# Kernel tuning notes

Measured on AMD Instinct MI355X. Metric: run time of the kernel, lower is better.

Reference implementation:

```python
import jax, jax.numpy as jnp
import numpy as np

B, T, C, H = 2, 2048, 1024, 16
HD = C // H  # head dim = 64


def setup_inputs() -> dict:
    key = jax.random.key(0)
    ks = jax.random.split(key, 5)
    s = 0.02
    return {
        "x": jax.random.normal(ks[0], (B, T, C), dtype=jnp.float32),
        "w_attn": jax.random.normal(ks[1], (C, 3 * C), dtype=jnp.float32) * s,
        "b_attn": jnp.zeros((3 * C,), dtype=jnp.float32),
        "w_proj": jax.random.normal(ks[2], (C, C), dtype=jnp.float32) * s,
        "b_proj": jnp.zeros((C,), dtype=jnp.float32),
    }


def reference(x, w_attn, b_attn, w_proj, b_proj):
    Bc, Tc, Cc = x.shape
    qkv = x @ w_attn + b_attn                      # [B,T,3C]
    q, k, v = jnp.split(qkv, 3, axis=2)            # each [B,T,C]
    # [B,T,C] -> [B,H,T,HD]
    def heads(t):
        return t.reshape(Bc, Tc, H, HD).transpose(0, 2, 1, 3)
    q, k, v = heads(q), heads(k), heads(v)
    scale = 1.0 / jnp.sqrt(jnp.asarray(HD, dtype=x.dtype))
    att = jnp.einsum("bhqd,bhkd->bhqk", q, k) * scale   # [B,H,T,T]
    causal = jnp.tril(jnp.ones((Tc, Tc), dtype=bool))
    att = jnp.where(causal, att, jnp.asarray(-jnp.inf, dtype=att.dtype))
    att = jax.nn.softmax(att, axis=-1)
    y = jnp.einsum("bhqk,bhkd->bhqd", att, v)            # [B,H,T,HD]
    y = y.transpose(0, 2, 1, 3).reshape(Bc, Tc, Cc)      # [B,T,C]
    return y @ w_proj + b_proj
```

## Files before the change

kernel.cpp:

```cpp
#include <hip/hip_runtime.h>
#include <stdint.h>


typedef short bf16x8 __attribute__((ext_vector_type(8)));
typedef float f32x4 __attribute__((ext_vector_type(4)));

__device__ inline unsigned short f2bf(float f) {
  union { float f; uint32_t u; } v; v.f = f;
  uint32_t u = v.u;
  u += 0x7FFFu + ((u >> 16) & 1u);
  return (unsigned short)(u >> 16);
}

__device__ inline unsigned pkbf(float a, float b) {
  unsigned r;
  asm("v_cvt_pk_bf16_f32 %0, %1, %2" : "=v"(r) : "v"(a), "v"(b));
  return r;
}

__device__ inline float exp2_fast(float x) {
#if __has_builtin(__builtin_amdgcn_exp2f)
  return __builtin_amdgcn_exp2f(x);
#else
  float r; asm("v_exp_f32 %0, %1" : "=v"(r) : "v"(x)); return r;
#endif
}

__device__ inline void load_lds16(const unsigned short* g, unsigned short* l) {
  __builtin_amdgcn_global_load_lds(
      (const __attribute__((address_space(1))) unsigned int*)(const void*)g,
      (__attribute__((address_space(3))) unsigned int*)(void*)l, 16, 0, 0);
}

__global__ __launch_bounds__(256) void prep_kernel(
    const float* __restrict__ x, const float* __restrict__ w_attn,
    const float* __restrict__ w_proj,
    unsigned short* __restrict__ xb, unsigned short* __restrict__ wattnT,
    unsigned short* __restrict__ wprojT) {
  __shared__ float tile[32][33];
  const int b = blockIdx.x, t = threadIdx.x;
  if (b < 4096) {
    int i = b * 256 + t;
    float4 f = reinterpret_cast<const float4*>(x)[i];
    ushort4 o;
    o.x = f2bf(f.x); o.y = f2bf(f.y); o.z = f2bf(f.z); o.w = f2bf(f.w);
    reinterpret_cast<ushort4*>(xb)[i] = o;
    return;
  }
  const float* in; unsigned short* out; int R, Cn, bx, by;
  if (b < 7168) {
    int bb = b - 4096;
    in = w_attn; out = wattnT; R = 1024; Cn = 3072;
    bx = (bb % 96) * 32; by = (bb / 96) * 32;
  } else {
    int bb = b - 7168;
    in = w_proj; out = wprojT; R = 1024; Cn = 1024;
    bx = (bb % 32) * 32; by = (bb / 32) * 32;
  }
  const int tx = t & 31, ty = t >> 5;
  #pragma unroll
  for (int i = 0; i < 32; i += 8)
    tile[ty + i][tx] = in[(size_t)(by + ty + i) * Cn + bx + tx];
  __syncthreads();
  #pragma unroll
  for (int i = 0; i < 32; i += 8)
    out[(size_t)(bx + ty + i) * R + by + tx] = f2bf(tile[tx][ty + i]);
}

__global__ __launch_bounds__(256) void gemm_bt64_kernel(
    const unsigned short* __restrict__ A,
    const unsigned short* __restrict__ Bt,
    const float* __restrict__ bias,
    void* __restrict__ outp,
    unsigned short* __restrict__ vtp,
    int M, int N, int K, int mode) {
  __shared__ unsigned short As[2][128 * 64];
  __shared__ unsigned short Bs[2][128 * 64];
  const int t = threadIdx.x;
  const int wave = t >> 6, lane = t & 63;
  const int L = lane & 15, quad = lane >> 4;
  const int wm = (wave >> 1) * 64, wn = (wave & 1) * 64;
  const int m0 = blockIdx.y * 128, n0 = blockIdx.x * 128;

  const int drow = lane >> 3;
  const int dch  = (lane & 7) ^ drow;
  const int fo0 = ((quad ^ (L & 7)) * 8);
  const int fo1 = (((quad + 4) ^ (L & 7)) * 8);

  const unsigned short* Ab = A  + (size_t)(m0 + wave * 32 + drow) * K + dch * 8;
  const unsigned short* Bb = Bt + (size_t)(n0 + wave * 32 + drow) * K + dch * 8;

  f32x4 acc[4][4] = {};
  const int NK2 = K >> 6;

  #pragma unroll
  for (int j = 0; j < 4; ++j) {
    int r0 = wave * 32 + j * 8;
    load_lds16(Ab + (size_t)j * 8 * K, &As[0][r0 * 64]);
    load_lds16(Bb + (size_t)j * 8 * K, &Bs[0][r0 * 64]);
  }

  int buf = 0;
  for (int kt = 0; kt < NK2; ++kt) {
    asm volatile("" ::: "memory");
    __builtin_amdgcn_s_waitcnt(0x0F70);
    __builtin_amdgcn_s_barrier();
    asm volatile("" ::: "memory");

    if (kt + 1 < NK2) {
      #pragma unroll
      for (int j = 0; j < 4; ++j) {
        int r0 = wave * 32 + j * 8;
        load_lds16(Ab + (size_t)j * 8 * K + (size_t)(kt + 1) * 64, &As[buf ^ 1][r0 * 64]);
        load_lds16(Bb + (size_t)j * 8 * K + (size_t)(kt + 1) * 64, &Bs[buf ^ 1][r0 * 64]);
      }
    }

    bf16x8 af[4], bf[4];
    #pragma unroll
    for (int mt = 0; mt < 4; ++mt)
      af[mt] = *reinterpret_cast<const bf16x8*>(&As[buf][(wm + mt * 16 + L) * 64 + fo0]);
    #pragma unroll
    for (int nt = 0; nt < 4; ++nt)
      bf[nt] = *reinterpret_cast<const bf16x8*>(&Bs[buf][(wn + nt * 16 + L) * 64 + fo0]);
    __builtin_amdgcn_s_setprio(1);
    #pragma unroll
    for (int mt = 0; mt < 4; ++mt)
      #pragma unroll
      for (int nt = 0; nt < 4; ++nt)
        acc[mt][nt] = __builtin_amdgcn_mfma_f32_16x16x32_bf16(af[mt], bf[nt], acc[mt][nt], 0, 0, 0);
    __builtin_amdgcn_s_setprio(0);

    #pragma unroll
    for (int mt = 0; mt < 4; ++mt)
      af[mt] = *reinterpret_cast<const bf16x8*>(&As[buf][(wm + mt * 16 + L) * 64 + fo1]);
    #pragma unroll
    for (int nt = 0; nt < 4; ++nt)
      bf[nt] = *reinterpret_cast<const bf16x8*>(&Bs[buf][(wn + nt * 16 + L) * 64 + fo1]);
    __builtin_amdgcn_s_setprio(1);
    #pragma unroll
    for (int mt = 0; mt < 4; ++mt)
      #pragma unroll
      for (int nt = 0; nt < 4; ++nt)
        acc[mt][nt] = __builtin_amdgcn_mfma_f32_16x16x32_bf16(af[mt], bf[nt], acc[mt][nt], 0, 0, 0);
    __builtin_amdgcn_s_setprio(0);
    buf ^= 1;
  }

  if (mode == 0) {
    float* out = (float*)outp;
    #pragma unroll
    for (int mt = 0; mt < 4; ++mt)
      #pragma unroll
      for (int nt = 0; nt < 4; ++nt) {
        int col = n0 + wn + nt * 16 + L;
        float b = bias[col];
        #pragma unroll
        for (int r = 0; r < 4; ++r) {
          int row = m0 + wm + mt * 16 + quad * 4 + r;
          out[(size_t)row * N + col] = acc[mt][nt][r] + b;
        }
      }
  } else {
    unsigned short* qkv = (unsigned short*)outp;
    #pragma unroll
    for (int mt = 0; mt < 4; ++mt)
      #pragma unroll
      for (int nt = 0; nt < 4; ++nt) {
        int col = n0 + wn + nt * 16 + L;
        int sel = col >> 10, cc = col & 1023;
        int h = cc >> 6, d = cc & 63;
        float b = bias[col];
        float sc = (sel == 0) ? 0.18033688011112042f : 1.0f;
        #pragma unroll
        for (int r = 0; r < 4; ++r) {
          int row = m0 + wm + mt * 16 + quad * 4 + r;
          int bb = row >> 11, tt = row & 2047;
          float val = (acc[mt][nt][r] + b) * sc;
          if (sel == 2) {
            vtp[((size_t)(bb * 16 + h) * 64 + d) * 2048 + tt] = f2bf(val);
          } else {
            qkv[(((size_t)sel * 32 + (size_t)(bb * 16 + h)) * 2048 + tt) * 64 + d] = f2bf(val);
          }
        }
      }
  }
}

template<int BM, int BN>
__global__ __launch_bounds__(256) void gemm_bt_kernel(
    const unsigned short* __restrict__ A,
    const unsigned short* __restrict__ Bt,
    const float* __restrict__ bias,
    float* __restrict__ out,
    int M, int N, int K) {
  constexpr int MT = BM / 32, NT = BN / 32;
  constexpr int RPWA = BM / 4, RPWB = BN / 4;
  constexpr int NJA = RPWA / 16, NJB = RPWB / 16;
  __shared__ unsigned short As[2][BM * 32];
  __shared__ unsigned short Bs[2][BN * 32];
  const int t = threadIdx.x;
  const int wave = t >> 6, lane = t & 63;
  const int L = lane & 15, quad = lane >> 4;
  const int wm = (wave >> 1) * (BM / 2), wn = (wave & 1) * (BN / 2);
  const int m0 = blockIdx.y * BM, n0 = blockIdx.x * BN;

  const int drow = lane >> 2;
  const int dch  = (lane & 3) ^ ((drow >> 1) & 3);
  const int foff = ((quad ^ ((L >> 1) & 3)) * 8);

  const unsigned short* Ab = A  + (size_t)(m0 + wave * RPWA + drow) * K + dch * 8;
  const unsigned short* Bb = Bt + (size_t)(n0 + wave * RPWB + drow) * K + dch * 8;

  f32x4 acc[MT][NT] = {};
  const int NK = K >> 5;

  #pragma unroll
  for (int j = 0; j < NJA; ++j)
    load_lds16(Ab + (size_t)j * 16 * K, &As[0][(wave * RPWA + j * 16) * 32]);
  #pragma unroll
  for (int j = 0; j < NJB; ++j)
    load_lds16(Bb + (size_t)j * 16 * K, &Bs[0][(wave * RPWB + j * 16) * 32]);

  int buf = 0;
  for (int kt = 0; kt < NK; ++kt) {
    asm volatile("" ::: "memory");
    __builtin_amdgcn_s_waitcnt(0x0F70);
    __builtin_amdgcn_s_barrier();
    asm volatile("" ::: "memory");

    if (kt + 1 < NK) {
      #pragma unroll
      for (int j = 0; j < NJA; ++j)
        load_lds16(Ab + (size_t)j * 16 * K + (kt + 1) * 32,
                   &As[buf ^ 1][(wave * RPWA + j * 16) * 32]);
      #pragma unroll
      for (int j = 0; j < NJB; ++j)
        load_lds16(Bb + (size_t)j * 16 * K + (kt + 1) * 32,
                   &Bs[buf ^ 1][(wave * RPWB + j * 16) * 32]);
    }

    bf16x8 af[MT], bf[NT];
    #pragma unroll
    for (int mt = 0; mt < MT; ++mt)
      af[mt] = *reinterpret_cast<const bf16x8*>(&As[buf][(wm + mt * 16 + L) * 32 + foff]);
    #pragma unroll
    for (int nt = 0; nt < NT; ++nt)
      bf[nt] = *reinterpret_cast<const bf16x8*>(&Bs[buf][(wn + nt * 16 + L) * 32 + foff]);
    __builtin_amdgcn_s_setprio(1);
    #pragma unroll
    for (int mt = 0; mt < MT; ++mt)
      #pragma unroll
      for (int nt = 0; nt < NT; ++nt)
        acc[mt][nt] = __builtin_amdgcn_mfma_f32_16x16x32_bf16(af[mt], bf[nt], acc[mt][nt], 0, 0, 0);
    __builtin_amdgcn_s_setprio(0);
    buf ^= 1;
  }

  #pragma unroll
  for (int mt = 0; mt < MT; ++mt)
    #pragma unroll
    for (int nt = 0; nt < NT; ++nt) {
      int col = n0 + wn + nt * 16 + L;
      float b = bias[col];
      #pragma unroll
      for (int r = 0; r < 4; ++r) {
        int row = m0 + wm + mt * 16 + quad * 4 + r;
        out[(size_t)row * N + col] = acc[mt][nt][r] + b;
      }
    }
}

__global__ __launch_bounds__(256) void attn_kernel(
    const unsigned short* __restrict__ qkv,
    const unsigned short* __restrict__ vt,
    unsigned short* __restrict__ y) {
  __shared__ unsigned short Ks[3][64 * 64];
  __shared__ unsigned short Vs[3][64 * 64];
  __shared__ unsigned short Ps[4][32][72];

  const int t = threadIdx.x;
  const int wave = t >> 6, lane = t & 63;
  const int L = lane & 15, quad = lane >> 4;
  const int b = blockIdx.x;
  const int bh = (b & 7) * 4 + ((b >> 3) & 3);
  const int pi = b >> 5;
  const int tA = pi, tB = 31 - pi;
  const int rowA0 = tA * 64 + wave * 16;
  const int rowB0 = tB * 64 + wave * 16;
  const int ntiles = tB + 1;

  const unsigned short* qb  = qkv + ((size_t)bh * 2048) * 64;
  const unsigned short* kb  = qkv + ((size_t)(32 + bh) * 2048) * 64;
  const unsigned short* vtb = vt + (size_t)bh * 64 * 2048;

  const int drow = lane >> 3;
  const int dch  = (lane & 7) ^ drow;
  const int fo0 = ((quad ^ (L & 7)) * 8);
  const int fo1 = (((quad + 4) ^ (L & 7)) * 8);

  bf16x8 qfA[2], qfB[2];
  #pragma unroll
  for (int h = 0; h < 2; ++h) {
    qfA[h] = *reinterpret_cast<const bf16x8*>(qb + (size_t)(rowA0 + L) * 64 + h * 32 + quad * 8);
    qfB[h] = *reinterpret_cast<const bf16x8*>(qb + (size_t)(rowB0 + L) * 64 + h * 32 + quad * 8);
  }

  f32x4 oA[4] = {}, oB[4] = {};
  float rsA = 0.f, rsB = 0.f;

  {
    #pragma unroll
    for (int j = 0; j < 2; ++j) {
      int r0 = wave * 16 + j * 8;
      load_lds16(kb  + (size_t)(0 + r0 + drow) * 64 + dch * 8, &Ks[0][r0 * 64]);
      load_lds16(vtb + (size_t)(r0 + drow) * 2048 + 0 + dch * 8, &Vs[0][r0 * 64]);
    }
  }

  int buf = 0;
  for (int kt = 0; kt < ntiles; ++kt) {
    const int nkt = (kt + 1 < ntiles) ? kt + 1 : ntiles - 1;
    const int nbuf = (buf == 2) ? 0 : buf + 1;
    {
      const int kg = nkt * 64;
      #pragma unroll
      for (int j = 0; j < 2; ++j) {
        int r0 = wave * 16 + j * 8;
        load_lds16(kb  + (size_t)(kg + r0 + drow) * 64 + dch * 8, &Ks[nbuf][r0 * 64]);
        load_lds16(vtb + (size_t)(r0 + drow) * 2048 + kg + dch * 8, &Vs[nbuf][r0 * 64]);
      }
    }
    asm volatile("" ::: "memory");
    __builtin_amdgcn_s_waitcnt(0x0F74);
    __builtin_amdgcn_s_barrier();
    asm volatile("" ::: "memory");

    const bool actA = (kt <= tA);

    bf16x8 kf[4][2];
    #pragma unroll
    for (int nt = 0; nt < 4; ++nt) {
      kf[nt][0] = *reinterpret_cast<const bf16x8*>(&Ks[buf][(nt * 16 + L) * 64 + fo0]);
      kf[nt][1] = *reinterpret_cast<const bf16x8*>(&Ks[buf][(nt * 16 + L) * 64 + fo1]);
    }

    f32x4 sB[4] = {};
    __builtin_amdgcn_s_setprio(1);
    #pragma unroll
    for (int nt = 0; nt < 4; ++nt) {
      sB[nt] = __builtin_amdgcn_mfma_f32_16x16x32_bf16(kf[nt][0], qfB[0], sB[nt], 0, 0, 0);
      sB[nt] = __builtin_amdgcn_mfma_f32_16x16x32_bf16(kf[nt][1], qfB[1], sB[nt], 0, 0, 0);
    }
    __builtin_amdgcn_s_setprio(0);
    if (kt == tB) {
      #pragma unroll
      for (int nt = 0; nt < 4; ++nt) {
        int key0 = kt * 64 + nt * 16 + quad * 4;
        int qr = rowB0 + L;
        #pragma unroll
        for (int r = 0; r < 4; ++r)
          if (key0 + r > qr) sB[nt][r] = -3.0e38f;
      }
    }
    #pragma unroll
    for (int nt = 0; nt < 4; ++nt) {
      float p0 = exp2_fast(sB[nt][0]), p1 = exp2_fast(sB[nt][1]);
      float p2 = exp2_fast(sB[nt][2]), p3 = exp2_fast(sB[nt][3]);
      rsB += (p0 + p1) + (p2 + p3);
      uint2 pk;
      pk.x = pkbf(p0, p1);
      pk.y = pkbf(p2, p3);
      *reinterpret_cast<uint2*>(&Ps[wave][16 + L][nt * 16 + quad * 4]) = pk;
    }

    if (actA) {
      f32x4 sA[4] = {};
      __builtin_amdgcn_s_setprio(1);
      #pragma unroll
      for (int nt = 0; nt < 4; ++nt) {
        sA[nt] = __builtin_amdgcn_mfma_f32_16x16x32_bf16(kf[nt][0], qfA[0], sA[nt], 0, 0, 0);
        sA[nt] = __builtin_amdgcn_mfma_f32_16x16x32_bf16(kf[nt][1], qfA[1], sA[nt], 0, 0, 0);
      }
      __builtin_amdgcn_s_setprio(0);
      if (kt == tA) {
        #pragma unroll
        for (int nt = 0; nt < 4; ++nt) {
          int key0 = kt * 64 + nt * 16 + quad * 4;
          int qr = rowA0 + L;
          #pragma unroll
          for (int r = 0; r < 4; ++r)
            if (key0 + r > qr) sA[nt][r] = -3.0e38f;
        }
      }
      #pragma unroll
      for (int nt = 0; nt < 4; ++nt) {
        float p0 = exp2_fast(sA[nt][0]), p1 = exp2_fast(sA[nt][1]);
        float p2 = exp2_fast(sA[nt][2]), p3 = exp2_fast(sA[nt][3]);
        rsA += (p0 + p1) + (p2 + p3);
        uint2 pk;
        pk.x = pkbf(p0, p1);
        pk.y = pkbf(p2, p3);
        *reinterpret_cast<uint2*>(&Ps[wave][L][nt * 16 + quad * 4]) = pk;
      }
    }

    bf16x8 vf[4][2];
    #pragma unroll
    for (int nt = 0; nt < 4; ++nt) {
      vf[nt][0] = *reinterpret_cast<const bf16x8*>(&Vs[buf][(nt * 16 + L) * 64 + fo0]);
      vf[nt][1] = *reinterpret_cast<const bf16x8*>(&Vs[buf][(nt * 16 + L) * 64 + fo1]);
    }
    bf16x8 pb0 = *reinterpret_cast<const bf16x8*>(&Ps[wave][16 + L][quad * 8]);
    bf16x8 pb1 = *reinterpret_cast<const bf16x8*>(&Ps[wave][16 + L][32 + quad * 8]);
    __builtin_amdgcn_s_setprio(1);
    #pragma unroll
    for (int nt = 0; nt < 4; ++nt) {
      oB[nt] = __builtin_amdgcn_mfma_f32_16x16x32_bf16(pb0, vf[nt][0], oB[nt], 0, 0, 0);
      oB[nt] = __builtin_amdgcn_mfma_f32_16x16x32_bf16(pb1, vf[nt][1], oB[nt], 0, 0, 0);
    }
    __builtin_amdgcn_s_setprio(0);
    if (actA) {
      bf16x8 pa0 = *reinterpret_cast<const bf16x8*>(&Ps[wave][L][quad * 8]);
      bf16x8 pa1 = *reinterpret_cast<const bf16x8*>(&Ps[wave][L][32 + quad * 8]);
      __builtin_amdgcn_s_setprio(1);
      #pragma unroll
      for (int nt = 0; nt < 4; ++nt) {
        oA[nt] = __builtin_amdgcn_mfma_f32_16x16x32_bf16(pa0, vf[nt][0], oA[nt], 0, 0, 0);
        oA[nt] = __builtin_amdgcn_mfma_f32_16x16x32_bf16(pa1, vf[nt][1], oA[nt], 0, 0, 0);
      }
      __builtin_amdgcn_s_setprio(0);
    }
    buf = nbuf;
  }

  float a = rsA; a += __shfl_xor(a, 16, 64); a += __shfl_xor(a, 32, 64);
  float b2 = rsB; b2 += __shfl_xor(b2, 16, 64); b2 += __shfl_xor(b2, 32, 64);
  float invA[4], invB[4];
  #pragma unroll
  for (int r = 0; r < 4; ++r) {
    invA[r] = 1.0f / __shfl(a, quad * 4 + r, 64);
    invB[r] = 1.0f / __shfl(b2, quad * 4 + r, 64);
  }
  const int bb = bh >> 4, hh = bh & 15;
  #pragma unroll
  for (int nt = 0; nt < 4; ++nt)
    #pragma unroll
    for (int r = 0; r < 4; ++r) {
      int rA = rowA0 + quad * 4 + r;
      int rB = rowB0 + quad * 4 + r;
      int col = hh * 64 + nt * 16 + L;
      y[((size_t)bb * 2048 + rA) * 1024 + col] = f2bf(oA[nt][r] * invA[r]);
      y[((size_t)bb * 2048 + rB) * 1024 + col] = f2bf(oB[nt][r] * invB[r]);
    }
  __builtin_amdgcn_s_waitcnt(0);
}

extern "C" void kernel_launch(void* const* d_in, const int* in_sizes, int n_in,
                              void* d_out, int out_size, void* d_ws, size_t ws_size,
                              hipStream_t stream) {
  const float* x      = (const float*)d_in[0];
  const float* w_attn = (const float*)d_in[1];
  const float* b_attn = (const float*)d_in[2];
  const float* w_proj = (const float*)d_in[3];
  const float* b_proj = (const float*)d_in[4];
  float* out = (float*)d_out;

  unsigned short* ws = (unsigned short*)d_ws;
  unsigned short* xb     = ws;
  unsigned short* wattnT = xb + 4194304;
  unsigned short* wprojT = wattnT + 3145728;
  unsigned short* qkv    = wprojT + 1048576;
  unsigned short* yb     = qkv + 12582912;
  unsigned short* vt     = yb + 4194304;

  prep_kernel<<<8192, 256, 0, stream>>>(x, w_attn, w_proj, xb, wattnT, wprojT);

  gemm_bt64_kernel<<<dim3(24, 32), 256, 0, stream>>>(xb, wattnT, b_attn, qkv, vt, 4096, 3072, 1024, 1);
  attn_kernel<<<dim3(512), 256, 0, stream>>>(qkv, vt, yb);
  gemm_bt_kernel<64, 64><<<dim3(16, 64), 256, 0, stream>>>(yb, wprojT, b_proj, out, 4096, 1024, 1024);
}
```

Baseline: 190.9 us.

## Fuse all stages into one cooperative persistent kernel with grid syncs

```diff
diff --git a/kernel.cpp b/kernel.cpp
--- a/kernel.cpp
+++ b/kernel.cpp
@@ -1,5 +1,8 @@
 #include <hip/hip_runtime.h>
+#include <hip/hip_cooperative_groups.h>
 #include <stdint.h>
+
+namespace cg = cooperative_groups;
 
 
 typedef short bf16x8 __attribute__((ext_vector_type(8)));
@@ -30,6 +33,367 @@
   __builtin_amdgcn_global_load_lds(
       (const __attribute__((address_space(1))) unsigned int*)(const void*)g,
       (__attribute__((address_space(3))) unsigned int*)(void*)l, 16, 0, 0);
+}
+
+__global__ __launch_bounds__(256, 2) void fused_all_kernel(
+    const float* __restrict__ x, const float* __restrict__ w_attn,
+    const float* __restrict__ bias_attn, const float* __restrict__ w_proj,
+    const float* __restrict__ bias_proj, float* __restrict__ out,
+    unsigned short* __restrict__ xb, unsigned short* __restrict__ wattnT,
+    unsigned short* __restrict__ wprojT, unsigned short* __restrict__ qkvp,
+    unsigned short* __restrict__ yb, unsigned short* __restrict__ vt) {
+  __shared__ __align__(16) unsigned char smem[67584];
+  cg::grid_group grid = cg::this_grid();
+  const int bid = blockIdx.x;
+  const int t = threadIdx.x;
+  const int wave = t >> 6, lane = t & 63;
+  const int L = lane & 15, quad = lane >> 4;
+
+  {
+    float (*tile)[33] = reinterpret_cast<float(*)[33]>(smem);
+    for (int u = bid; u < 8192; u += 512) {
+      if (u < 4096) {
+        int i = u * 256 + t;
+        float4 f = reinterpret_cast<const float4*>(x)[i];
+        ushort4 o;
+        o.x = f2bf(f.x); o.y = f2bf(f.y); o.z = f2bf(f.z); o.w = f2bf(f.w);
+        reinterpret_cast<ushort4*>(xb)[i] = o;
+        continue;
+      }
+      const float* in; unsigned short* outp2; int R, Cn, bx, by;
+      if (u < 7168) {
+        int bb = u - 4096;
+        in = w_attn; outp2 = wattnT; R = 1024; Cn = 3072;
+        bx = (bb % 96) * 32; by = (bb / 96) * 32;
+      } else {
+        int bb = u - 7168;
+        in = w_proj; outp2 = wprojT; R = 1024; Cn = 1024;
+        bx = (bb % 32) * 32; by = (bb / 32) * 32;
+      }
+      const int tx = t & 31, ty = t >> 5;
+      __syncthreads();
+      #pragma unroll
+      for (int i = 0; i < 32; i += 8)
+        tile[ty + i][tx] = in[(size_t)(by + ty + i) * Cn + bx + tx];
+      __syncthreads();
+      #pragma unroll
+      for (int i = 0; i < 32; i += 8)
+        outp2[(size_t)(bx + ty + i) * R + by + tx] = f2bf(tile[tx][ty + i]);
+    }
+  }
+  grid.sync();
+
+  {
+    constexpr int K = 1024;
+    unsigned short (*As)[128 * 32] = reinterpret_cast<unsigned short(*)[128 * 32]>(smem);
+    unsigned short (*Bs)[128 * 32] = reinterpret_cast<unsigned short(*)[128 * 32]>(smem + 16384);
+    const int wm = (wave >> 1) * 64, wn = (wave & 1) * 64;
+    const int drow = lane >> 2;
+    const int dch  = (lane & 3) ^ ((drow >> 1) & 3);
+    const int foff = ((quad ^ ((L >> 1) & 3)) * 8);
+
+    for (int u = bid; u < 768; u += 512) {
+      const int m0 = (u / 24) * 128, n0 = (u % 24) * 128;
+      const unsigned short* Ab = xb     + (size_t)(m0 + wave * 32 + drow) * K + dch * 8;
+      const unsigned short* Bb = wattnT + (size_t)(n0 + wave * 32 + drow) * K + dch * 8;
+      f32x4 acc[4][4] = {};
+
+      #pragma unroll
+      for (int j = 0; j < 2; ++j) {
+        load_lds16(Ab + (size_t)j * 16 * K, &As[0][(wave * 32 + j * 16) * 32]);
+        load_lds16(Bb + (size_t)j * 16 * K, &Bs[0][(wave * 32 + j * 16) * 32]);
+      }
+      int buf = 0;
+      for (int kt = 0; kt < 32; ++kt) {
+        asm volatile("" ::: "memory");
+        __builtin_amdgcn_s_waitcnt(0x0F70);
+        __builtin_amdgcn_s_barrier();
+        asm volatile("" ::: "memory");
+        if (kt + 1 < 32) {
+          #pragma unroll
+          for (int j = 0; j < 2; ++j) {
+            load_lds16(Ab + (size_t)j * 16 * K + (kt + 1) * 32,
+                       &As[buf ^ 1][(wave * 32 + j * 16) * 32]);
+            load_lds16(Bb + (size_t)j * 16 * K + (kt + 1) * 32,
+                       &Bs[buf ^ 1][(wave * 32 + j * 16) * 32]);
+          }
+        }
+        bf16x8 af[4], bf[4];
+        #pragma unroll
+        for (int mt = 0; mt < 4; ++mt)
+          af[mt] = *reinterpret_cast<const bf16x8*>(&As[buf][(wm + mt * 16 + L) * 32 + foff]);
+        #pragma unroll
+        for (int nt = 0; nt < 4; ++nt)
+          bf[nt] = *reinterpret_cast<const bf16x8*>(&Bs[buf][(wn + nt * 16 + L) * 32 + foff]);
+        __builtin_amdgcn_s_setprio(1);
+        #pragma unroll
+        for (int mt = 0; mt < 4; ++mt)
+          #pragma unroll
+          for (int nt = 0; nt < 4; ++nt)
+            acc[mt][nt] = __builtin_amdgcn_mfma_f32_16x16x32_bf16(af[mt], bf[nt], acc[mt][nt], 0, 0, 0);
+        __builtin_amdgcn_s_setprio(0);
+        buf ^= 1;
+      }
+      #pragma unroll
+      for (int mt = 0; mt < 4; ++mt)
+        #pragma unroll
+        for (int nt = 0; nt < 4; ++nt) {
+          int col = n0 + wn + nt * 16 + L;
+          int sel = col >> 10, cc = col & 1023;
+          int h = cc >> 6, d = cc & 63;
+          float b = bias_attn[col];
+          float sc = (sel == 0) ? 0.18033688011112042f : 1.0f;
+          #pragma unroll
+          for (int r = 0; r < 4; ++r) {
+            int row = m0 + wm + mt * 16 + quad * 4 + r;
+            int bb = row >> 11, tt = row & 2047;
+            float val = (acc[mt][nt][r] + b) * sc;
+            if (sel == 2) {
+              vt[((size_t)(bb * 16 + h) * 64 + d) * 2048 + tt] = f2bf(val);
+            } else {
+              qkvp[(((size_t)sel * 32 + (size_t)(bb * 16 + h)) * 2048 + tt) * 64 + d] = f2bf(val);
+            }
+          }
+        }
+    }
+  }
+  grid.sync();
+
+  {
+    unsigned short (*Ks)[64 * 64] = reinterpret_cast<unsigned short(*)[64 * 64]>(smem);
+    unsigned short (*Vs)[64 * 64] = reinterpret_cast<unsigned short(*)[64 * 64]>(smem + 24576);
+    unsigned short (*Ps)[32][72]  = reinterpret_cast<unsigned short(*)[32][72]>(smem + 49152);
+
+    const int b = bid;
+    const int bh = (b & 7) * 4 + ((b >> 3) & 3);
+    const int pi = b >> 5;
+    const int tA = pi, tB = 31 - pi;
+    const int rowA0 = tA * 64 + wave * 16;
+    const int rowB0 = tB * 64 + wave * 16;
+    const int ntiles = tB + 1;
+
+    const unsigned short* qb  = qkvp + ((size_t)bh * 2048) * 64;
+    const unsigned short* kb  = qkvp + ((size_t)(32 + bh) * 2048) * 64;
+    const unsigned short* vtb = vt + (size_t)bh * 64 * 2048;
+
+    const int drow = lane >> 3;
+    const int dch  = (lane & 7) ^ drow;
+    const int fo0 = ((quad ^ (L & 7)) * 8);
+    const int fo1 = (((quad + 4) ^ (L & 7)) * 8);
+
+    bf16x8 qfA[2], qfB[2];
+    #pragma unroll
+    for (int h = 0; h < 2; ++h) {
+      qfA[h] = *reinterpret_cast<const bf16x8*>(qb + (size_t)(rowA0 + L) * 64 + h * 32 + quad * 8);
+      qfB[h] = *reinterpret_cast<const bf16x8*>(qb + (size_t)(rowB0 + L) * 64 + h * 32 + quad * 8);
+    }
+
+    f32x4 oA[4] = {}, oB[4] = {};
+    float rsA = 0.f, rsB = 0.f;
+
+    #pragma unroll
+    for (int j = 0; j < 2; ++j) {
+      int r0 = wave * 16 + j * 8;
+      load_lds16(kb  + (size_t)(r0 + drow) * 64 + dch * 8, &Ks[0][r0 * 64]);
+      load_lds16(vtb + (size_t)(r0 + drow) * 2048 + dch * 8, &Vs[0][r0 * 64]);
+    }
+
+    int buf = 0;
+    for (int kt = 0; kt < ntiles; ++kt) {
+      const int nkt = (kt + 1 < ntiles) ? kt + 1 : ntiles - 1;
+      const int nbuf = (buf == 2) ? 0 : buf + 1;
+      {
+        const int kg = nkt * 64;
+        #pragma unroll
+        for (int j = 0; j < 2; ++j) {
+          int r0 = wave * 16 + j * 8;
+          load_lds16(kb  + (size_t)(kg + r0 + drow) * 64 + dch * 8, &Ks[nbuf][r0 * 64]);
+          load_lds16(vtb + (size_t)(r0 + drow) * 2048 + kg + dch * 8, &Vs[nbuf][r0 * 64]);
+        }
+      }
+      asm volatile("" ::: "memory");
+      __builtin_amdgcn_s_waitcnt(0x0F74);
+      __builtin_amdgcn_s_barrier();
+      asm volatile("" ::: "memory");
+
+      const bool actA = (kt <= tA);
+
+      bf16x8 kf[4][2];
+      #pragma unroll
+      for (int nt = 0; nt < 4; ++nt) {
+        kf[nt][0] = *reinterpret_cast<const bf16x8*>(&Ks[buf][(nt * 16 + L) * 64 + fo0]);
+        kf[nt][1] = *reinterpret_cast<const bf16x8*>(&Ks[buf][(nt * 16 + L) * 64 + fo1]);
+      }
+
+      f32x4 sB[4] = {};
+      __builtin_amdgcn_s_setprio(1);
+      #pragma unroll
+      for (int nt = 0; nt < 4; ++nt) {
+        sB[nt] = __builtin_amdgcn_mfma_f32_16x16x32_bf16(kf[nt][0], qfB[0], sB[nt], 0, 0, 0);
+        sB[nt] = __builtin_amdgcn_mfma_f32_16x16x32_bf16(kf[nt][1], qfB[1], sB[nt], 0, 0, 0);
+      }
+      __builtin_amdgcn_s_setprio(0);
+      if (kt == tB) {
+        #pragma unroll
+        for (int nt = 0; nt < 4; ++nt) {
+          int key0 = kt * 64 + nt * 16 + quad * 4;
+          int qr = rowB0 + L;
+          #pragma unroll
+          for (int r = 0; r < 4; ++r)
+            if (key0 + r > qr) sB[nt][r] = -3.0e38f;
+        }
+      }
+      #pragma unroll
+      for (int nt = 0; nt < 4; ++nt) {
+        float p0 = exp2_fast(sB[nt][0]), p1 = exp2_fast(sB[nt][1]);
+        float p2 = exp2_fast(sB[nt][2]), p3 = exp2_fast(sB[nt][3]);
+        rsB += (p0 + p1) + (p2 + p3);
+        uint2 pk;
+        pk.x = pkbf(p0, p1);
+        pk.y = pkbf(p2, p3);
+        *reinterpret_cast<uint2*>(&Ps[wave][16 + L][nt * 16 + quad * 4]) = pk;
+      }
+
+      if (actA) {
+        f32x4 sA[4] = {};
+        __builtin_amdgcn_s_setprio(1);
+        #pragma unroll
+        for (int nt = 0; nt < 4; ++nt) {
+          sA[nt] = __builtin_amdgcn_mfma_f32_16x16x32_bf16(kf[nt][0], qfA[0], sA[nt], 0, 0, 0);
+          sA[nt] = __builtin_amdgcn_mfma_f32_16x16x32_bf16(kf[nt][1], qfA[1], sA[nt], 0, 0, 0);
+        }
+        __builtin_amdgcn_s_setprio(0);
+        if (kt == tA) {
+          #pragma unroll
+          for (int nt = 0; nt < 4; ++nt) {
+            int key0 = kt * 64 + nt * 16 + quad * 4;
+            int qr = rowA0 + L;
+            #pragma unroll
+            for (int r = 0; r < 4; ++r)
+              if (key0 + r > qr) sA[nt][r] = -3.0e38f;
+          }
+        }
+        #pragma unroll
+        for (int nt = 0; nt < 4; ++nt) {
+          float p0 = exp2_fast(sA[nt][0]), p1 = exp2_fast(sA[nt][1]);
+          float p2 = exp2_fast(sA[nt][2]), p3 = exp2_fast(sA[nt][3]);
+          rsA += (p0 + p1) + (p2 + p3);
+          uint2 pk;
+          pk.x = pkbf(p0, p1);
+          pk.y = pkbf(p2, p3);
+          *reinterpret_cast<uint2*>(&Ps[wave][L][nt * 16 + quad * 4]) = pk;
+        }
+      }
+
+      bf16x8 vf[4][2];
+      #pragma unroll
+      for (int nt = 0; nt < 4; ++nt) {
+        vf[nt][0] = *reinterpret_cast<const bf16x8*>(&Vs[buf][(nt * 16 + L) * 64 + fo0]);
+        vf[nt][1] = *reinterpret_cast<const bf16x8*>(&Vs[buf][(nt * 16 + L) * 64 + fo1]);
+      }
+      bf16x8 pb0 = *reinterpret_cast<const bf16x8*>(&Ps[wave][16 + L][quad * 8]);
+      bf16x8 pb1 = *reinterpret_cast<const bf16x8*>(&Ps[wave][16 + L][32 + quad * 8]);
+      __builtin_amdgcn_s_setprio(1);
+      #pragma unroll
+      for (int nt = 0; nt < 4; ++nt) {
+        oB[nt] = __builtin_amdgcn_mfma_f32_16x16x32_bf16(pb0, vf[nt][0], oB[nt], 0, 0, 0);
+        oB[nt] = __builtin_amdgcn_mfma_f32_16x16x32_bf16(pb1, vf[nt][1], oB[nt], 0, 0, 0);
+      }
+      __builtin_amdgcn_s_setprio(0);
+      if (actA) {
+        bf16x8 pa0 = *reinterpret_cast<const bf16x8*>(&Ps[wave][L][quad * 8]);
+        bf16x8 pa1 = *reinterpret_cast<const bf16x8*>(&Ps[wave][L][32 + quad * 8]);
+        __builtin_amdgcn_s_setprio(1);
+        #pragma unroll
+        for (int nt = 0; nt < 4; ++nt) {
+          oA[nt] = __builtin_amdgcn_mfma_f32_16x16x32_bf16(pa0, vf[nt][0], oA[nt], 0, 0, 0);
+          oA[nt] = __builtin_amdgcn_mfma_f32_16x16x32_bf16(pa1, vf[nt][1], oA[nt], 0, 0, 0);
+        }
+        __builtin_amdgcn_s_setprio(0);
+      }
+      buf = nbuf;
+    }
+
+    float a = rsA; a += __shfl_xor(a, 16, 64); a += __shfl_xor(a, 32, 64);
+    float b2 = rsB; b2 += __shfl_xor(b2, 16, 64); b2 += __shfl_xor(b2, 32, 64);
+    float invA[4], invB[4];
+    #pragma unroll
+    for (int r = 0; r < 4; ++r) {
+      invA[r] = 1.0f / __shfl(a, quad * 4 + r, 64);
+      invB[r] = 1.0f / __shfl(b2, quad * 4 + r, 64);
+    }
+    const int bb = bh >> 4, hh = bh & 15;
+    #pragma unroll
+    for (int nt = 0; nt < 4; ++nt)
+      #pragma unroll
+      for (int r = 0; r < 4; ++r) {
+        int rA = rowA0 + quad * 4 + r;
+        int rB = rowB0 + quad * 4 + r;
+        int col = hh * 64 + nt * 16 + L;
+        yb[((size_t)bb * 2048 + rA) * 1024 + col] = f2bf(oA[nt][r] * invA[r]);
+        yb[((size_t)bb * 2048 + rB) * 1024 + col] = f2bf(oB[nt][r] * invB[r]);
+      }
+    __builtin_amdgcn_s_waitcnt(0);
+  }
+  grid.sync();
+
+  {
+    constexpr int K = 1024;
+    unsigned short (*As)[64 * 32] = reinterpret_cast<unsigned short(*)[64 * 32]>(smem);
+    unsigned short (*Bs)[64 * 32] = reinterpret_cast<unsigned short(*)[64 * 32]>(smem + 8192);
+    const int wm = (wave >> 1) * 32, wn = (wave & 1) * 32;
+    const int drow = lane >> 2;
+    const int dch  = (lane & 3) ^ ((drow >> 1) & 3);
+    const int foff = ((quad ^ ((L >> 1) & 3)) * 8);
+
+    for (int u = bid; u < 1024; u += 512) {
+      const int m0 = (u >> 4) * 64, n0 = (u & 15) * 64;
+      const unsigned short* Ab = yb     + (size_t)(m0 + wave * 16 + drow) * K + dch * 8;
+      const unsigned short* Bb = wprojT + (size_t)(n0 + wave * 16 + drow) * K + dch * 8;
+      f32x4 acc[2][2] = {};
+
+      load_lds16(Ab, &As[0][(wave * 16) * 32]);
+      load_lds16(Bb, &Bs[0][(wave * 16) * 32]);
+      int buf = 0;
+      for (int kt = 0; kt < 32; ++kt) {
+        asm volatile("" ::: "memory");
+        __builtin_amdgcn_s_waitcnt(0x0F70);
+        __builtin_amdgcn_s_barrier();
+        asm volatile("" ::: "memory");
+        if (kt + 1 < 32) {
+          load_lds16(Ab + (kt + 1) * 32, &As[buf ^ 1][(wave * 16) * 32]);
+          load_lds16(Bb + (kt + 1) * 32, &Bs[buf ^ 1][(wave * 16) * 32]);
+        }
+        bf16x8 af[2], bf[2];
+        #pragma unroll
+        for (int mt = 0; mt < 2; ++mt)
+          af[mt] = *reinterpret_cast<const bf16x8*>(&As[buf][(wm + mt * 16 + L) * 32 + foff]);
+        #pragma unroll
+        for (int nt = 0; nt < 2; ++nt)
+          bf[nt] = *reinterpret_cast<const bf16x8*>(&Bs[buf][(wn + nt * 16 + L) * 32 + foff]);
+        __builtin_amdgcn_s_setprio(1);
+        #pragma unroll
+        for (int mt = 0; mt < 2; ++mt)
+          #pragma unroll
+          for (int nt = 0; nt < 2; ++nt)
+            acc[mt][nt] = __builtin_amdgcn_mfma_f32_16x16x32_bf16(af[mt], bf[nt], acc[mt][nt], 0, 0, 0);
+        __builtin_amdgcn_s_setprio(0);
+        buf ^= 1;
+      }
+      #pragma unroll
+      for (int mt = 0; mt < 2; ++mt)
+        #pragma unroll
+        for (int nt = 0; nt < 2; ++nt) {
+          int col = n0 + wn + nt * 16 + L;
+          float b = bias_proj[col];
+          #pragma unroll
+          for (int r = 0; r < 4; ++r) {
+            int row = m0 + wm + mt * 16 + quad * 4 + r;
+            out[(size_t)row * 1024 + col] = acc[mt][nt][r] + b;
+          }
+        }
+    }
+  }
 }
 
 __global__ __launch_bounds__(256) void prep_kernel(
@@ -67,133 +431,14 @@
     out[(size_t)(bx + ty + i) * R + by + tx] = f2bf(tile[tx][ty + i]);
 }
 
-__global__ __launch_bounds__(256) void gemm_bt64_kernel(
+template<int BM, int BN>
+__global__ __launch_bounds__(256) void gemm_bt_kernel(
     const unsigned short* __restrict__ A,
     const unsigned short* __restrict__ Bt,
     const float* __restrict__ bias,
     void* __restrict__ outp,
     unsigned short* __restrict__ vtp,
     int M, int N, int K, int mode) {
-  __shared__ unsigned short As[2][128 * 64];
-  __shared__ unsigned short Bs[2][128 * 64];
-  const int t = threadIdx.x;
-  const int wave = t >> 6, lane = t & 63;
-  const int L = lane & 15, quad = lane >> 4;
-  const int wm = (wave >> 1) * 64, wn = (wave & 1) * 64;
-  const int m0 = blockIdx.y * 128, n0 = blockIdx.x * 128;
-
-  const int drow = lane >> 3;
-  const int dch  = (lane & 7) ^ drow;
-  const int fo0 = ((quad ^ (L & 7)) * 8);
-  const int fo1 = (((quad + 4) ^ (L & 7)) * 8);
-
-  const unsigned short* Ab = A  + (size_t)(m0 + wave * 32 + drow) * K + dch * 8;
-  const unsigned short* Bb = Bt + (size_t)(n0 + wave * 32 + drow) * K + dch * 8;
-
-  f32x4 acc[4][4] = {};
-  const int NK2 = K >> 6;
-
-  #pragma unroll
-  for (int j = 0; j < 4; ++j) {
-    int r0 = wave * 32 + j * 8;
-    load_lds16(Ab + (size_t)j * 8 * K, &As[0][r0 * 64]);
-    load_lds16(Bb + (size_t)j * 8 * K, &Bs[0][r0 * 64]);
-  }
-
-  int buf = 0;
-  for (int kt = 0; kt < NK2; ++kt) {
-    asm volatile("" ::: "memory");
-    __builtin_amdgcn_s_waitcnt(0x0F70);
-    __builtin_amdgcn_s_barrier();
-    asm volatile("" ::: "memory");
-
-    if (kt + 1 < NK2) {
-      #pragma unroll
-      for (int j = 0; j < 4; ++j) {
-        int r0 = wave * 32 + j * 8;
-        load_lds16(Ab + (size_t)j * 8 * K + (size_t)(kt + 1) * 64, &As[buf ^ 1][r0 * 64]);
-        load_lds16(Bb + (size_t)j * 8 * K + (size_t)(kt + 1) * 64, &Bs[buf ^ 1][r0 * 64]);
-      }
-    }
-
-    bf16x8 af[4], bf[4];
-    #pragma unroll
-    for (int mt = 0; mt < 4; ++mt)
-      af[mt] = *reinterpret_cast<const bf16x8*>(&As[buf][(wm + mt * 16 + L) * 64 + fo0]);
-    #pragma unroll
-    for (int nt = 0; nt < 4; ++nt)
-      bf[nt] = *reinterpret_cast<const bf16x8*>(&Bs[buf][(wn + nt * 16 + L) * 64 + fo0]);
-    __builtin_amdgcn_s_setprio(1);
-    #pragma unroll
-    for (int mt = 0; mt < 4; ++mt)
-      #pragma unroll
-      for (int nt = 0; nt < 4; ++nt)
-        acc[mt][nt] = __builtin_amdgcn_mfma_f32_16x16x32_bf16(af[mt], bf[nt], acc[mt][nt], 0, 0, 0);
-    __builtin_amdgcn_s_setprio(0);
-
-    #pragma unroll
-    for (int mt = 0; mt < 4; ++mt)
-      af[mt] = *reinterpret_cast<const bf16x8*>(&As[buf][(wm + mt * 16 + L) * 64 + fo1]);
-    #pragma unroll
-    for (int nt = 0; nt < 4; ++nt)
-      bf[nt] = *reinterpret_cast<const bf16x8*>(&Bs[buf][(wn + nt * 16 + L) * 64 + fo1]);
-    __builtin_amdgcn_s_setprio(1);
-    #pragma unroll
-    for (int mt = 0; mt < 4; ++mt)
-      #pragma unroll
-      for (int nt = 0; nt < 4; ++nt)
-        acc[mt][nt] = __builtin_amdgcn_mfma_f32_16x16x32_bf16(af[mt], bf[nt], acc[mt][nt], 0, 0, 0);
-    __builtin_amdgcn_s_setprio(0);
-    buf ^= 1;
-  }
-
-  if (mode == 0) {
-    float* out = (float*)outp;
-    #pragma unroll
-    for (int mt = 0; mt < 4; ++mt)
-      #pragma unroll
-      for (int nt = 0; nt < 4; ++nt) {
-        int col = n0 + wn + nt * 16 + L;
-        float b = bias[col];
-        #pragma unroll
-        for (int r = 0; r < 4; ++r) {
-          int row = m0 + wm + mt * 16 + quad * 4 + r;
-          out[(size_t)row * N + col] = acc[mt][nt][r] + b;
-        }
-      }
-  } else {
-    unsigned short* qkv = (unsigned short*)outp;
-    #pragma unroll
-    for (int mt = 0; mt < 4; ++mt)
-      #pragma unroll
-      for (int nt = 0; nt < 4; ++nt) {
-        int col = n0 + wn + nt * 16 + L;
-        int sel = col >> 10, cc = col & 1023;
-        int h = cc >> 6, d = cc & 63;
-        float b = bias[col];
-        float sc = (sel == 0) ? 0.18033688011112042f : 1.0f;
-        #pragma unroll
-        for (int r = 0; r < 4; ++r) {
-          int row = m0 + wm + mt * 16 + quad * 4 + r;
-          int bb = row >> 11, tt = row & 2047;
-          float val = (acc[mt][nt][r] + b) * sc;
-          if (sel == 2) {
-            vtp[((size_t)(bb * 16 + h) * 64 + d) * 2048 + tt] = f2bf(val);
-          } else {
-            qkv[(((size_t)sel * 32 + (size_t)(bb * 16 + h)) * 2048 + tt) * 64 + d] = f2bf(val);
-          }
-        }
-      }
-  }
-}
-
-template<int BM, int BN>
-__global__ __launch_bounds__(256) void gemm_bt_kernel(
-    const unsigned short* __restrict__ A,
-    const unsigned short* __restrict__ Bt,
-    const float* __restrict__ bias,
-    float* __restrict__ out,
-    int M, int N, int K) {
   constexpr int MT = BM / 32, NT = BN / 32;
   constexpr int RPWA = BM / 4, RPWB = BN / 4;
   constexpr int NJA = RPWA / 16, NJB = RPWB / 16;
@@ -257,18 +502,44 @@
     buf ^= 1;
   }
 
-  #pragma unroll
-  for (int mt = 0; mt < MT; ++mt)
-    #pragma unroll
-    for (int nt = 0; nt < NT; ++nt) {
-      int col = n0 + wn + nt * 16 + L;
-      float b = bias[col];
-      #pragma unroll
-      for (int r = 0; r < 4; ++r) {
-        int row = m0 + wm + mt * 16 + quad * 4 + r;
-        out[(size_t)row * N + col] = acc[mt][nt][r] + b;
-      }
-    }
+  if (mode == 0) {
+    float* out = (float*)outp;
+    #pragma unroll
+    for (int mt = 0; mt < MT; ++mt)
+      #pragma unroll
+      for (int nt = 0; nt < NT; ++nt) {
+        int col = n0 + wn + nt * 16 + L;
+        float b = bias[col];
+        #pragma unroll
+        for (int r = 0; r < 4; ++r) {
+          int row = m0 + wm + mt * 16 + quad * 4 + r;
+          out[(size_t)row * N + col] = acc[mt][nt][r] + b;
+        }
+      }
+  } else {
+    unsigned short* qkv = (unsigned short*)outp;
+    #pragma unroll
+    for (int mt = 0; mt < MT; ++mt)
+      #pragma unroll
+      for (int nt = 0; nt < NT; ++nt) {
+        int col = n0 + wn + nt * 16 + L;
+        int sel = col >> 10, cc = col & 1023;
+        int h = cc >> 6, d = cc & 63;
+        float b = bias[col];
+        float sc = (sel == 0) ? 0.18033688011112042f : 1.0f;
+        #pragma unroll
+        for (int r = 0; r < 4; ++r) {
+          int row = m0 + wm + mt * 16 + quad * 4 + r;
+          int bb = row >> 11, tt = row & 2047;
+          float val = (acc[mt][nt][r] + b) * sc;
+          if (sel == 2) {
+            vtp[((size_t)(bb * 16 + h) * 64 + d) * 2048 + tt] = f2bf(val);
+          } else {
+            qkv[(((size_t)sel * 32 + (size_t)(bb * 16 + h)) * 2048 + tt) * 64 + d] = f2bf(val);
+          }
+        }
+      }
+  }
 }
 
 __global__ __launch_bounds__(256) void attn_kernel(
@@ -474,9 +745,18 @@
   unsigned short* yb     = qkv + 12582912;
   unsigned short* vt     = yb + 4194304;
 
-  prep_kernel<<<8192, 256, 0, stream>>>(x, w_attn, w_proj, xb, wattnT, wprojT);
-
-  gemm_bt64_kernel<<<dim3(24, 32), 256, 0, stream>>>(xb, wattnT, b_attn, qkv, vt, 4096, 3072, 1024, 1);
-  attn_kernel<<<dim3(512), 256, 0, stream>>>(qkv, vt, yb);
-  gemm_bt_kernel<64, 64><<<dim3(16, 64), 256, 0, stream>>>(yb, wprojT, b_proj, out, 4096, 1024, 1024);
-}
+  void* args[] = {
+    (void*)&x, (void*)&w_attn, (void*)&b_attn, (void*)&w_proj, (void*)&b_proj,
+    (void*)&out, (void*)&xb, (void*)&wattnT, (void*)&wprojT, (void*)&qkv,
+    (void*)&yb, (void*)&vt
+  };
+  hipError_t err = hipLaunchCooperativeKernel(
+      reinterpret_cast<void*>(fused_all_kernel), dim3(512), dim3(256), args, 0, stream);
+  if (err != hipSuccess) {
+    (void)hipGetLastError();
+    prep_kernel<<<8192, 256, 0, stream>>>(x, w_attn, w_proj, xb, wattnT, wprojT);
+    gemm_bt_kernel<128, 128><<<dim3(24, 32), 256, 0, stream>>>(xb, wattnT, b_attn, qkv, vt, 4096, 3072, 1024, 1);
+    attn_kernel<<<dim3(512), 256, 0, stream>>>(qkv, vt, yb);
+    gemm_bt_kernel<64, 64><<<dim3(16, 64), 256, 0, stream>>>(yb, wprojT, b_proj, out, nullptr, 4096, 1024, 1024, 0);
+  }
+}
```

Result: slower. 396.1 us (+107.4%).
